# Performance work log

Measured on AMD Instinct MI355X. Metric: run time of the kernel, lower is better.

The kernel has to match this reference:

```python
import jax, jax.numpy as jnp
import numpy as np

B, C, P, D = 4096, 1000, 10, 256
N = C * P            # total prototypes
E = 160000           # edges among prototypes
MARGIN = -0.1
LOSS_WEIGHT = 0.1
EPS = 1e-12          # F.normalize eps


def _gcn_conv(x, src, dst, deg_isqrt, w, b):
    # PyG GCNConv: symmetric-normalized aggregation with self-loops (added by caller)
    xw = x @ w                                   # [N, D]
    norm = deg_isqrt[src] * deg_isqrt[dst]       # [E+N]
    msg = norm[:, None] * xw[src]                # [E+N, D]
    out = jax.ops.segment_sum(msg, dst, num_segments=N)
    return out + b


def setup_inputs() -> dict:
    key = jax.random.key(0)
    ks = jax.random.split(key, 8)
    return {
        "hidden": jax.random.normal(ks[0], (B, D), jnp.float32),
        "labels": jax.random.randint(ks[1], (B,), 0, C),
        "edge_index": jax.random.randint(ks[2], (2, E), 0, N),
        "node_features": 0.02 * jax.random.normal(ks[3], (N, D), jnp.float32),
        "w1": jax.random.normal(ks[4], (D, D), jnp.float32) / np.sqrt(D),
        "b1": jnp.zeros((D,), jnp.float32),
        "w2": jax.random.normal(ks[5], (D, D), jnp.float32) / np.sqrt(D),
        "b2": jnp.zeros((D,), jnp.float32),
    }


def reference(hidden, labels, edge_index, node_features, w1, b1, w2, b2):
    # --- PrototypeGCN over the prototype graph (self-loops + sym norm) ---
    loops = jnp.arange(N, dtype=edge_index.dtype)
    src = jnp.concatenate([edge_index[0], loops])
    dst = jnp.concatenate([edge_index[1], loops])
    deg = jax.ops.segment_sum(jnp.ones_like(dst, jnp.float32), dst, num_segments=N)
    deg_isqrt = jnp.where(deg > 0, jax.lax.rsqrt(jnp.maximum(deg, 1.0)), 0.0)
    x = node_features
    x = jax.nn.relu(_gcn_conv(x, src, dst, deg_isqrt, w1, b1))
    x = jax.nn.relu(_gcn_conv(x, src, dst, deg_isqrt, w2, b2))

    # --- cosine similarity, per-class max over prototypes ---
    hidden_norm = hidden / jnp.maximum(jnp.linalg.norm(hidden, axis=1, keepdims=True), EPS)
    proto_norm = x / jnp.maximum(jnp.linalg.norm(x, axis=1, keepdims=True), EPS)
    sim = (1.0 + hidden_norm @ proto_norm.T) / 2.0          # [B, N]
    sim_pc = sim.reshape(B, C, P)
    output = sim_pc.max(axis=2)                              # [B, C]
    topk_idx = sim_pc.argmax(axis=2)                         # [B, C]

    # --- margin-masked cross entropy ---
    ar = jnp.arange(B)
    true_scores = output[ar, labels]
    pred_labels = output.argmax(axis=1)
    pred_scores = output.max(axis=1)
    mask = (true_scores - pred_scores) > MARGIN              # [B] bool
    cnt = mask.sum()
    per_ce = -jax.nn.log_softmax(output, axis=1)[ar, labels]
    ce_loss = jnp.sum(per_ce * mask) / jnp.maximum(cnt, 1).astype(per_ce.dtype)

    # dispersion = -mean(proto_norm @ proto_norm.T) = -||sum_i p_i||^2 / N^2
    s = proto_norm.sum(axis=0)
    dispersion_loss = -(s @ s) / (N * N)
    total_loss = jnp.where(cnt == 0, 0.0, ce_loss + LOSS_WEIGHT * dispersion_loss)

    # --- vectorized usage scatter (replaces Python double loop) ---
    pos_ids = labels * P + topk_idx[ar, labels]
    positive_usage = jnp.zeros((N,), jnp.float32).at[pos_ids].add(1.0)
    wrong = (pred_labels != labels).astype(jnp.float32)
    neg_ids = pred_labels * P + topk_idx[ar, pred_labels]
    negative_usage = jnp.zeros((N,), jnp.float32).at[neg_ids].add(wrong)

    return (output, total_loss, positive_usage, negative_usage)
```

## Files before the change

### kernel.cpp

```cpp
#include <hip/hip_runtime.h>
#include <math.h>

#define B_  4096
#define C_  1000
#define P_  10
#define D_  256
#define N_  10000
#define E_  160000

typedef __attribute__((ext_vector_type(8))) short short8;
typedef __attribute__((ext_vector_type(4))) float floatx4;

#define MFMA16(a, b, c) __builtin_amdgcn_mfma_f32_16x16x32_bf16((a), (b), (c), 0, 0, 0)

__device__ __forceinline__ float waveReduceSum(float v){
  #pragma unroll
  for (int o = 32; o > 0; o >>= 1) v += __shfl_xor(v, o);
  return v;
}
__device__ __forceinline__ unsigned short f2bf(float f){
  unsigned int u = __float_as_uint(f);
  unsigned int r = (u + 0x7FFFu + ((u >> 16) & 1u)) >> 16;
  return (unsigned short)r;
}
__device__ __forceinline__ float bf2f(unsigned short b){
  return __uint_as_float(((unsigned int)b) << 16);
}
__device__ __forceinline__ void gload_lds16(const void* g, void* l){
  __builtin_amdgcn_global_load_lds((const __attribute__((address_space(1))) void*)g,
                                   (__attribute__((address_space(3))) void*)l, 16, 0, 0);
}

__global__ void k_prep(const int* __restrict__ src, const int* __restrict__ dst,
                       int* __restrict__ cursor, int* __restrict__ csr_src,
                       const float* __restrict__ w1, const float* __restrict__ w2,
                       unsigned short* __restrict__ w1h, unsigned short* __restrict__ w1l,
                       unsigned short* __restrict__ w2h, unsigned short* __restrict__ w2l,
                       float* __restrict__ zero_zone,
                       const float* __restrict__ nodef,
                       unsigned short* __restrict__ NFh, unsigned short* __restrict__ NFl,
                       const float* __restrict__ hidden,
                       unsigned short* __restrict__ HNh, unsigned short* __restrict__ HNl){
  int b = blockIdx.x;
  int t = threadIdx.x;
  if (b < 625){
    int e = b * 256 + t;
    if (e < E_){
      int d = dst[e];
      int p = atomicAdd(&cursor[d], 1);
      p = (p < 63) ? p : 63;
      csr_src[d * 64 + p] = src[e];
    }
  } else if (b < 1137){
    int bb = b - 625;
    const float* w = (bb < 256) ? w1 : w2;
    int n = bb & 255;
    float x = w[(size_t)t * 256 + n];
    unsigned short h = f2bf(x);
    unsigned short l = f2bf(x - bf2f(h));
    if (bb < 256){ w1h[(size_t)n * 256 + t] = h; w1l[(size_t)n * 256 + t] = l; }
    else         { w2h[(size_t)n * 256 + t] = h; w2l[(size_t)n * 256 + t] = l; }
  } else if (b < 1216){
    int i = (b - 1137) * 256 + t;
    if (i < 1 + 2 * N_) zero_zone[i] = 0.f;
  } else if (b < 11216){
    size_t i = (size_t)(b - 1216) * 256 + t;
    float x = nodef[i];
    unsigned short h = f2bf(x);
    NFh[i] = h;
    NFl[i] = f2bf(x - bf2f(h));
  } else {
    int r = b - 11216;
    float v = hidden[(size_t)r * 256 + t];
    float ss = waveReduceSum(v * v);
    __shared__ float red[4];
    int w = t >> 6;
    if ((t & 63) == 0) red[w] = ss;
    __syncthreads();
    float tot = red[0] + red[1] + red[2] + red[3];
    float nrm = fmaxf(sqrtf(tot), 1e-12f);
    float x = v / nrm;
    unsigned short h = f2bf(x);
    HNh[(size_t)r * 256 + t] = h;
    HNl[(size_t)r * 256 + t] = f2bf(x - bf2f(h));
  }
}

__global__ __launch_bounds__(64) void k_gemm_mfma(
    const unsigned short* __restrict__ Ah, const unsigned short* __restrict__ Al,
    const unsigned short* __restrict__ Wh, const unsigned short* __restrict__ Wl,
    float* __restrict__ outp){
  int lane = threadIdx.x;
  int l15 = lane & 15, lq = lane >> 4;
  int rb = blockIdx.x * 64;
  int nb = blockIdx.y * 32;

  floatx4 acc[4][2];
  #pragma unroll
  for (int mt = 0; mt < 4; ++mt)
    #pragma unroll
    for (int nt = 0; nt < 2; ++nt) acc[mt][nt] = (floatx4){0.f,0.f,0.f,0.f};

  int arow[4];
  #pragma unroll
  for (int mt = 0; mt < 4; ++mt){
    int r = rb + mt * 16 + l15;
    arow[mt] = (r < N_) ? r : (N_ - 1);
  }
  for (int kc = 0; kc < 256; kc += 32){
    short8 ah[4], al[4], bh[2], bl[2];
    #pragma unroll
    for (int mt = 0; mt < 4; ++mt){
      size_t o = (size_t)arow[mt] * 256 + kc + lq * 8;
      ah[mt] = *(const short8*)(Ah + o);
      al[mt] = *(const short8*)(Al + o);
    }
    #pragma unroll
    for (int nt = 0; nt < 2; ++nt){
      size_t o = (size_t)(nb + nt * 16 + l15) * 256 + kc + lq * 8;
      bh[nt] = *(const short8*)(Wh + o);
      bl[nt] = *(const short8*)(Wl + o);
    }
    #pragma unroll
    for (int nt = 0; nt < 2; ++nt)
      #pragma unroll
      for (int mt = 0; mt < 4; ++mt) acc[mt][nt] = MFMA16(al[mt], bh[nt], acc[mt][nt]);
    #pragma unroll
    for (int nt = 0; nt < 2; ++nt)
      #pragma unroll
      for (int mt = 0; mt < 4; ++mt) acc[mt][nt] = MFMA16(ah[mt], bl[nt], acc[mt][nt]);
    #pragma unroll
    for (int nt = 0; nt < 2; ++nt)
      #pragma unroll
      for (int mt = 0; mt < 4; ++mt) acc[mt][nt] = MFMA16(ah[mt], bh[nt], acc[mt][nt]);
  }
  #pragma unroll
  for (int mt = 0; mt < 4; ++mt)
    #pragma unroll
    for (int r = 0; r < 4; ++r){
      int row = rb + mt * 16 + lq * 4 + r;
      if (row < N_){
        #pragma unroll
        for (int nt = 0; nt < 2; ++nt)
          outp[(size_t)row * 256 + nb + nt * 16 + l15] = acc[mt][nt][r];
      }
    }
}

__global__ void k_agg_split(const float* __restrict__ XW, const int* __restrict__ deg,
                            const int* __restrict__ csr_src,
                            const float* __restrict__ bias,
                            unsigned short* __restrict__ Xh, unsigned short* __restrict__ Xl){
  int n    = blockIdx.x * 4 + (threadIdx.x >> 6);
  int lane = threadIdx.x & 63;
  int c4   = lane * 4;
  int dgn = deg[n];
  int dg = (dgn < 64) ? dgn : 64;
  int   esr = (lane < dg) ? csr_src[n * 64 + lane] : 0;
  float is  = 1.0f / sqrtf((float)(dgn + 1));
  float en  = (1.0f / sqrtf((float)(deg[esr] + 1))) * is;
  float4 s = *(const float4*)(XW + (size_t)n * 256 + c4);
  float w = is * is;
  float4 a = make_float4(w * s.x, w * s.y, w * s.z, w * s.w);
  int i = 0;
  for (; i + 3 < dg; i += 4){
    int s0 = __shfl(esr, i),   s1 = __shfl(esr, i+1), s2 = __shfl(esr, i+2), s3 = __shfl(esr, i+3);
    float n0 = __shfl(en, i),  n1 = __shfl(en, i+1),  n2 = __shfl(en, i+2),  n3 = __shfl(en, i+3);
    float4 v0 = *(const float4*)(XW + (size_t)s0 * 256 + c4);
    float4 v1 = *(const float4*)(XW + (size_t)s1 * 256 + c4);
    float4 v2 = *(const float4*)(XW + (size_t)s2 * 256 + c4);
    float4 v3 = *(const float4*)(XW + (size_t)s3 * 256 + c4);
    a.x += n0*v0.x + n1*v1.x + n2*v2.x + n3*v3.x;
    a.y += n0*v0.y + n1*v1.y + n2*v2.y + n3*v3.y;
    a.z += n0*v0.z + n1*v1.z + n2*v2.z + n3*v3.z;
    a.w += n0*v0.w + n1*v1.w + n2*v2.w + n3*v3.w;
  }
  for (; i < dg; ++i){
    int s0 = __shfl(esr, i); float n0 = __shfl(en, i);
    float4 v0 = *(const float4*)(XW + (size_t)s0 * 256 + c4);
    a.x += n0 * v0.x; a.y += n0 * v0.y; a.z += n0 * v0.z; a.w += n0 * v0.w;
  }
  float4 b = *(const float4*)(bias + c4);
  float x0 = fmaxf(a.x + b.x, 0.f), x1 = fmaxf(a.y + b.y, 0.f);
  float x2 = fmaxf(a.z + b.z, 0.f), x3 = fmaxf(a.w + b.w, 0.f);
  unsigned short h0 = f2bf(x0), h1 = f2bf(x1), h2 = f2bf(x2), h3 = f2bf(x3);
  ushort4 hv = make_ushort4(h0, h1, h2, h3);
  ushort4 lv = make_ushort4(f2bf(x0 - bf2f(h0)), f2bf(x1 - bf2f(h1)),
                            f2bf(x2 - bf2f(h2)), f2bf(x3 - bf2f(h3)));
  *(ushort4*)(Xh + (size_t)n * 256 + c4) = hv;
  *(ushort4*)(Xl + (size_t)n * 256 + c4) = lv;
}

__global__ void k_agg_norm_split(const float* __restrict__ XW, const int* __restrict__ deg,
                                 const int* __restrict__ csr_src,
                                 const float* __restrict__ bias,
                                 unsigned short* __restrict__ Ph, unsigned short* __restrict__ Pl){
  int n    = blockIdx.x * 4 + (threadIdx.x >> 6);
  int lane = threadIdx.x & 63;
  int c4   = lane * 4;
  int dgn = deg[n];
  int dg = (dgn < 64) ? dgn : 64;
  int   esr = (lane < dg) ? csr_src[n * 64 + lane] : 0;
  float is  = 1.0f / sqrtf((float)(dgn + 1));
  float en  = (1.0f / sqrtf((float)(deg[esr] + 1))) * is;
  float4 s = *(const float4*)(XW + (size_t)n * 256 + c4);
  float w = is * is;
  float4 a = make_float4(w * s.x, w * s.y, w * s.z, w * s.w);
  int i = 0;
  for (; i + 3 < dg; i += 4){
    int s0 = __shfl(esr, i),   s1 = __shfl(esr, i+1), s2 = __shfl(esr, i+2), s3 = __shfl(esr, i+3);
    float n0 = __shfl(en, i),  n1 = __shfl(en, i+1),  n2 = __shfl(en, i+2),  n3 = __shfl(en, i+3);
    float4 v0 = *(const float4*)(XW + (size_t)s0 * 256 + c4);
    float4 v1 = *(const float4*)(XW + (size_t)s1 * 256 + c4);
    float4 v2 = *(const float4*)(XW + (size_t)s2 * 256 + c4);
    float4 v3 = *(const float4*)(XW + (size_t)s3 * 256 + c4);
    a.x += n0*v0.x + n1*v1.x + n2*v2.x + n3*v3.x;
    a.y += n0*v0.y + n1*v1.y + n2*v2.y + n3*v3.y;
    a.z += n0*v0.z + n1*v1.z + n2*v2.z + n3*v3.z;
    a.w += n0*v0.w + n1*v1.w + n2*v2.w + n3*v3.w;
  }
  for (; i < dg; ++i){
    int s0 = __shfl(esr, i); float n0 = __shfl(en, i);
    float4 v0 = *(const float4*)(XW + (size_t)s0 * 256 + c4);
    a.x += n0 * v0.x; a.y += n0 * v0.y; a.z += n0 * v0.z; a.w += n0 * v0.w;
  }
  float4 b = *(const float4*)(bias + c4);
  float x0 = fmaxf(a.x + b.x, 0.f), x1 = fmaxf(a.y + b.y, 0.f);
  float x2 = fmaxf(a.z + b.z, 0.f), x3 = fmaxf(a.w + b.w, 0.f);
  float ss = x0*x0 + x1*x1 + x2*x2 + x3*x3;
  float tot = waveReduceSum(ss);
  float nrm = fmaxf(sqrtf(tot), 1e-12f);
  x0 /= nrm; x1 /= nrm; x2 /= nrm; x3 /= nrm;
  unsigned short h0 = f2bf(x0), h1 = f2bf(x1), h2 = f2bf(x2), h3 = f2bf(x3);
  ushort4 hv = make_ushort4(h0, h1, h2, h3);
  ushort4 lv = make_ushort4(f2bf(x0 - bf2f(h0)), f2bf(x1 - bf2f(h1)),
                            f2bf(x2 - bf2f(h2)), f2bf(x3 - bf2f(h3)));
  *(ushort4*)(Ph + (size_t)n * 256 + c4) = hv;
  *(ushort4*)(Pl + (size_t)n * 256 + c4) = lv;
}

__global__ void k_colsum(const unsigned short* __restrict__ hi,
                         const unsigned short* __restrict__ lo,
                         float* __restrict__ s){
  int d = threadIdx.x;
  int r0 = blockIdx.x * 100;
  float acc = 0.f;
  for (int r = r0; r < r0 + 100; ++r)
    acc += bf2f(hi[(size_t)r * 256 + d]) + bf2f(lo[(size_t)r * 256 + d]);
  atomicAdd(&s[d], acc);
}

__global__ __launch_bounds__(256, 4) void k_sim_max(
    const unsigned short* __restrict__ HNh, const unsigned short* __restrict__ HNl,
    const unsigned short* __restrict__ PNh, const unsigned short* __restrict__ PNl,
    float* __restrict__ out, unsigned char* __restrict__ idxb){
  __shared__ __align__(16) char smem[20736];

  int tid  = threadIdx.x;
  int wid  = tid >> 6;
  int lane = tid & 63;
  int l15  = lane & 15, lq = lane >> 4;
  int rbw  = blockIdx.y * 128 + wid * 32;
  int cb80 = blockIdx.x * 80;

  int swz  = (l15 >> 1) & 3;
  int srow = lane >> 2;
  int skq  = (lane & 3) ^ ((lane >> 3) & 3);

  floatx4 acc[2][5];
  #pragma unroll
  for (int mt = 0; mt < 2; ++mt)
    #pragma unroll
    for (int nt = 0; nt < 5; ++nt) acc[mt][nt] = (floatx4){0.f,0.f,0.f,0.f};

  const unsigned short* a0h = HNh + (size_t)(rbw + l15) * 256 + lq * 8;
  const unsigned short* a0l = HNl + (size_t)(rbw + l15) * 256 + lq * 8;

  auto stage1 = [&](int kc, int pb, int c){
    int bsel = (c >= 5) ? 1 : 0;
    int s = c - bsel * 5;
    int row = s * 16 + srow;
    const unsigned short* gp = (bsel ? PNl : PNh)
        + (size_t)(cb80 + row) * 256 + kc + skq * 8;
    char* lp = smem + pb * 10240 + bsel * 5120 + s * 1024;
    gload_lds16(gp, lp);
  };
  auto stageAll = [&](int kc, int pb){
    stage1(kc, pb, wid);
    stage1(kc, pb, wid + 4);
    if (wid < 2) stage1(kc, pb, wid + 8);
  };

  stageAll(0, 0);
  short8 ah[2], al[2];
  #pragma unroll
  for (int mt = 0; mt < 2; ++mt){
    ah[mt] = *(const short8*)(a0h + (size_t)mt * 4096);
    al[mt] = *(const short8*)(a0l + (size_t)mt * 4096);
  }
  __syncthreads();

  int p = 0;
  for (int kc = 0; kc < 256; kc += 32){
    const unsigned short* Bh = (const unsigned short*)(smem + p * 10240);
    const unsigned short* Bl = Bh + 2560;
    short8 ah2[2], al2[2];
    if (kc < 224){
      stageAll(kc + 32, p ^ 1);
      #pragma unroll
      for (int mt = 0; mt < 2; ++mt){
        ah2[mt] = *(const short8*)(a0h + (size_t)mt * 4096 + kc + 32);
        al2[mt] = *(const short8*)(a0l + (size_t)mt * 4096 + kc + 32);
      }
    }
    {
      int r0 = (0 * 16 + l15) * 32 + (lq ^ swz) * 8;
      int r1 = (1 * 16 + l15) * 32 + (lq ^ swz) * 8;
      int r2 = (2 * 16 + l15) * 32 + (lq ^ swz) * 8;
      short8 bh0 = *(const short8*)(Bh + r0), bl0 = *(const short8*)(Bl + r0);
      short8 bh1 = *(const short8*)(Bh + r1), bl1 = *(const short8*)(Bl + r1);
      short8 bh2 = *(const short8*)(Bh + r2), bl2 = *(const short8*)(Bl + r2);
      acc[0][0] = MFMA16(al[0], bh0, acc[0][0]);
      acc[1][0] = MFMA16(al[1], bh0, acc[1][0]);
      acc[0][1] = MFMA16(al[0], bh1, acc[0][1]);
      acc[1][1] = MFMA16(al[1], bh1, acc[1][1]);
      acc[0][2] = MFMA16(al[0], bh2, acc[0][2]);
      acc[1][2] = MFMA16(al[1], bh2, acc[1][2]);
      acc[0][0] = MFMA16(ah[0], bl0, acc[0][0]);
      acc[1][0] = MFMA16(ah[1], bl0, acc[1][0]);
      acc[0][1] = MFMA16(ah[0], bl1, acc[0][1]);
      acc[1][1] = MFMA16(ah[1], bl1, acc[1][1]);
      acc[0][2] = MFMA16(ah[0], bl2, acc[0][2]);
      acc[1][2] = MFMA16(ah[1], bl2, acc[1][2]);
      acc[0][0] = MFMA16(ah[0], bh0, acc[0][0]);
      acc[1][0] = MFMA16(ah[1], bh0, acc[1][0]);
      acc[0][1] = MFMA16(ah[0], bh1, acc[0][1]);
      acc[1][1] = MFMA16(ah[1], bh1, acc[1][1]);
      acc[0][2] = MFMA16(ah[0], bh2, acc[0][2]);
      acc[1][2] = MFMA16(ah[1], bh2, acc[1][2]);
    }
    {
      int r3 = (3 * 16 + l15) * 32 + (lq ^ swz) * 8;
      int r4 = (4 * 16 + l15) * 32 + (lq ^ swz) * 8;
      short8 bh3 = *(const short8*)(Bh + r3), bl3 = *(const short8*)(Bl + r3);
      short8 bh4 = *(const short8*)(Bh + r4), bl4 = *(const short8*)(Bl + r4);
      acc[0][3] = MFMA16(al[0], bh3, acc[0][3]);
      acc[1][3] = MFMA16(al[1], bh3, acc[1][3]);
      acc[0][4] = MFMA16(al[0], bh4, acc[0][4]);
      acc[1][4] = MFMA16(al[1], bh4, acc[1][4]);
      acc[0][3] = MFMA16(ah[0], bl3, acc[0][3]);
      acc[1][3] = MFMA16(ah[1], bl3, acc[1][3]);
      acc[0][4] = MFMA16(ah[0], bl4, acc[0][4]);
      acc[1][4] = MFMA16(ah[1], bl4, acc[1][4]);
      acc[0][3] = MFMA16(ah[0], bh3, acc[0][3]);
      acc[1][3] = MFMA16(ah[1], bh3, acc[1][3]);
      acc[0][4] = MFMA16(ah[0], bh4, acc[0][4]);
      acc[1][4] = MFMA16(ah[1], bh4, acc[1][4]);
    }
    ah[0] = ah2[0]; ah[1] = ah2[1];
    al[0] = al2[0]; al[1] = al2[1];
    __syncthreads();
    p ^= 1;
  }

  float* redw = (float*)smem + wid * 1296;
  #pragma unroll
  for (int mt = 0; mt < 2; ++mt){
    #pragma unroll
    for (int nt = 0; nt < 5; ++nt)
      #pragma unroll
      for (int r = 0; r < 4; ++r)
        redw[(lq * 4 + r) * 81 + nt * 16 + l15] = acc[mt][nt][r];
    int row = lane >> 2;
    int q   = lane & 3;
    const float* basep = redw + row * 81 + q * 20;
    float vs[2]; int is[2];
    #pragma unroll
    for (int cc = 0; cc < 2; ++cc){
      float m = 0.5f * (1.0f + basep[cc * 10]); int mi = 0;
      #pragma unroll
      for (int p2 = 1; p2 < 10; ++p2){
        float v = 0.5f * (1.0f + basep[cc * 10 + p2]);
        if (v > m){ m = v; mi = p2; }
      }
      vs[cc] = m; is[cc] = mi;
    }
    int grow = rbw + mt * 16 + row;
    int gcol = blockIdx.x * 8 + q * 2;
    *(float2*)(out + (size_t)grow * 1000 + gcol) = make_float2(vs[0], vs[1]);
    idxb[(size_t)grow * 1000 + gcol]     = (unsigned char)is[0];
    idxb[(size_t)grow * 1000 + gcol + 1] = (unsigned char)is[1];
  }
}

__global__ void k_row_pass(const float* __restrict__ out, const unsigned char* __restrict__ idxb,
                           const int* __restrict__ labels, int* __restrict__ cnt,
                           float* __restrict__ ce_sum, float* __restrict__ pos_usage,
                           float* __restrict__ neg_usage){
  int b = blockIdx.x * 4 + (threadIdx.x >> 6);
  int lane = threadIdx.x & 63;
  const float* row = out + (size_t)b * 1000;
  float v[16];
  #pragma unroll
  for (int j = 0; j < 4; ++j){
    int f4 = j * 64 + lane;
    if (f4 < 250){
      float4 t = *(const float4*)(row + f4 * 4);
      v[j*4+0] = t.x; v[j*4+1] = t.y; v[j*4+2] = t.z; v[j*4+3] = t.w;
    } else {
      v[j*4+0] = v[j*4+1] = v[j*4+2] = v[j*4+3] = -INFINITY;
    }
  }
  float m = -INFINITY; int mi = 0x7fffffff;
  #pragma unroll
  for (int j = 0; j < 4; ++j)
    #pragma unroll
    for (int k = 0; k < 4; ++k){
      float x = v[j*4+k];
      if (x > m){ m = x; mi = (j * 64 + lane) * 4 + k; }
    }
  #pragma unroll
  for (int o = 32; o > 0; o >>= 1){
    float m2 = __shfl_xor(m, o);
    int   i2 = __shfl_xor(mi, o);
    if (m2 > m || (m2 == m && i2 < mi)){ m = m2; mi = i2; }
  }
  float s = 0.f;
  #pragma unroll
  for (int t = 0; t < 16; ++t) s += __expf(v[t] - m);
  s = waveReduceSum(s);
  if (lane == 0){
    int lab = labels[b];
    float true_score = row[lab];
    float per_ce = m + __logf(s) - true_score;
    bool mask = (true_score - m) > -0.1f;
    if (mask){ atomicAdd(cnt, 1); atomicAdd(ce_sum, per_ce); }
    int pi = idxb[(size_t)b * 1000 + lab];
    atomicAdd(&pos_usage[lab * P_ + pi], 1.f);
    if (mi != lab){
      int ni = idxb[(size_t)b * 1000 + mi];
      atomicAdd(&neg_usage[mi * P_ + ni], 1.f);
    }
  }
}

__global__ void k_finalize(const float* __restrict__ s, const int* __restrict__ cnt,
                           const float* __restrict__ ce_sum, float* __restrict__ loss_out){
  int t = threadIdx.x;
  float v = s[t];
  float ss = waveReduceSum(v * v);
  __shared__ float red[4];
  if ((t & 63) == 0) red[t >> 6] = ss;
  __syncthreads();
  if (t == 0){
    float tot = red[0] + red[1] + red[2] + red[3];
    float disp = -tot / 1.0e8f;
    int c = *cnt;
    float total = (c == 0) ? 0.f
                : (*ce_sum / (float)(c < 1 ? 1 : c) + 0.1f * disp);
    *loss_out = total;
  }
}

extern "C" void kernel_launch(void* const* d_in, const int* in_sizes, int n_in,
                              void* d_out, int out_size, void* d_ws, size_t ws_size,
                              hipStream_t stream){
  const float* hidden = (const float*)d_in[0];
  const int*   labels = (const int*)  d_in[1];
  const int*   eidx   = (const int*)  d_in[2];
  const float* nodef  = (const float*)d_in[3];
  const float* w1     = (const float*)d_in[4];
  const float* b1     = (const float*)d_in[5];
  const float* w2     = (const float*)d_in[6];
  const float* b2     = (const float*)d_in[7];

  float* out       = (float*)d_out;
  float* loss_out  = out + (size_t)B_ * C_;
  float* pos_usage = loss_out + 1;
  float* neg_usage = pos_usage + N_;

  const int* srcp = eidx;
  const int* dstp = eidx + E_;

  char* base = (char*)d_ws;
  size_t off = 0;
  auto alloc = [&](size_t bytes) -> char* {
    char* p = base + off;
    off = (off + bytes + 255) & ~(size_t)255;
    return p;
  };
  int*   cursor  = (int*)  alloc((size_t)N_ * 4);
  float* svec    = (float*)alloc(256 * 4);
  int*   cnt     = (int*)  alloc(4);
  float* ce_sum  = (float*)alloc(4);
  size_t zero_bytes = off;
  int*   csr_src   = (int*)  alloc((size_t)N_ * 64 * 4);
  float* XW        = (float*)alloc((size_t)N_ * 256 * 4);
  unsigned short* NFh = (unsigned short*)alloc((size_t)N_ * 256 * 2);
  unsigned short* NFl = (unsigned short*)alloc((size_t)N_ * 256 * 2);
  unsigned short* Xh  = (unsigned short*)alloc((size_t)N_ * 256 * 2);
  unsigned short* Xl  = (unsigned short*)alloc((size_t)N_ * 256 * 2);
  unsigned short* Ph  = (unsigned short*)alloc((size_t)N_ * 256 * 2);
  unsigned short* Pl  = (unsigned short*)alloc((size_t)N_ * 256 * 2);
  unsigned short* W1h = (unsigned short*)alloc(256 * 256 * 2);
  unsigned short* W1l = (unsigned short*)alloc(256 * 256 * 2);
  unsigned short* W2h = (unsigned short*)alloc(256 * 256 * 2);
  unsigned short* W2l = (unsigned short*)alloc(256 * 256 * 2);
  unsigned short* HNh = (unsigned short*)alloc((size_t)B_ * 256 * 2);
  unsigned short* HNl = (unsigned short*)alloc((size_t)B_ * 256 * 2);
  unsigned char* idxb = (unsigned char*)alloc((size_t)B_ * C_);

  hipMemsetAsync(base, 0, zero_bytes, stream);

  k_prep<<<15312, 256, 0, stream>>>(srcp, dstp, cursor, csr_src,
                                    w1, w2, W1h, W1l, W2h, W2l, loss_out,
                                    nodef, NFh, NFl, hidden, HNh, HNl);

  dim3 ggrid(157, 8);
  k_gemm_mfma<<<ggrid, 64, 0, stream>>>(NFh, NFl, W1h, W1l, XW);
  k_agg_split<<<N_ / 4, 256, 0, stream>>>(XW, cursor, csr_src, b1, Xh, Xl);
  k_gemm_mfma<<<ggrid, 64, 0, stream>>>(Xh, Xl, W2h, W2l, XW);
  k_agg_norm_split<<<N_ / 4, 256, 0, stream>>>(XW, cursor, csr_src, b2, Ph, Pl);

  k_colsum<<<100, 256, 0, stream>>>(Ph, Pl, svec);

  dim3 sgrid(125, 32);
  k_sim_max<<<sgrid, 256, 0, stream>>>(HNh, HNl, Ph, Pl, out, idxb);

  k_row_pass<<<B_ / 4, 256, 0, stream>>>(out, idxb, labels, cnt, ce_sum, pos_usage, neg_usage);
  k_finalize<<<1, 256, 0, stream>>>(svec, cnt, ce_sum, loss_out);
}
```

Baseline: 334.3 us.

## Unroll gather by eight, swizzle sim_max block order, fold colsum into row pass

The aggregation loops now gather eight neighbour rows per iteration into two independent accumulators, so more loads are in flight and the add dependency chain is shorter. k_sim_max moves from a 2D grid to a 1D grid that is remapped into 16x16 block tiles, so blocks running at the same time share prototype and hidden tiles in L2. The launches over the padding range exit early. The separate column-sum kernel is folded into k_row_pass as 100 extra blocks, which removes one launch. The trade-offs are more registers per thread in the aggregation and wasted early-exit blocks in the sim grid.

```diff
diff --git a/kernel.cpp b/kernel.cpp
--- a/kernel.cpp
+++ b/kernel.cpp
@@ -162,24 +162,29 @@
   float4 s = *(const float4*)(XW + (size_t)n * 256 + c4);
   float w = is * is;
   float4 a = make_float4(w * s.x, w * s.y, w * s.z, w * s.w);
+  float4 a2 = make_float4(0.f, 0.f, 0.f, 0.f);
   int i = 0;
-  for (; i + 3 < dg; i += 4){
-    int s0 = __shfl(esr, i),   s1 = __shfl(esr, i+1), s2 = __shfl(esr, i+2), s3 = __shfl(esr, i+3);
-    float n0 = __shfl(en, i),  n1 = __shfl(en, i+1),  n2 = __shfl(en, i+2),  n3 = __shfl(en, i+3);
-    float4 v0 = *(const float4*)(XW + (size_t)s0 * 256 + c4);
-    float4 v1 = *(const float4*)(XW + (size_t)s1 * 256 + c4);
-    float4 v2 = *(const float4*)(XW + (size_t)s2 * 256 + c4);
-    float4 v3 = *(const float4*)(XW + (size_t)s3 * 256 + c4);
-    a.x += n0*v0.x + n1*v1.x + n2*v2.x + n3*v3.x;
-    a.y += n0*v0.y + n1*v1.y + n2*v2.y + n3*v3.y;
-    a.z += n0*v0.z + n1*v1.z + n2*v2.z + n3*v3.z;
-    a.w += n0*v0.w + n1*v1.w + n2*v2.w + n3*v3.w;
+  for (; i + 7 < dg; i += 8){
+    int   si[8]; float ni[8];
+    #pragma unroll
+    for (int j = 0; j < 8; ++j){ si[j] = __shfl(esr, i+j); ni[j] = __shfl(en, i+j); }
+    float4 vv[8];
+    #pragma unroll
+    for (int j = 0; j < 8; ++j) vv[j] = *(const float4*)(XW + (size_t)si[j] * 256 + c4);
+    #pragma unroll
+    for (int j = 0; j < 4; ++j){
+      a.x  += ni[j]   * vv[j].x;   a.y  += ni[j]   * vv[j].y;
+      a.z  += ni[j]   * vv[j].z;   a.w  += ni[j]   * vv[j].w;
+      a2.x += ni[j+4] * vv[j+4].x; a2.y += ni[j+4] * vv[j+4].y;
+      a2.z += ni[j+4] * vv[j+4].z; a2.w += ni[j+4] * vv[j+4].w;
+    }
   }
   for (; i < dg; ++i){
     int s0 = __shfl(esr, i); float n0 = __shfl(en, i);
     float4 v0 = *(const float4*)(XW + (size_t)s0 * 256 + c4);
     a.x += n0 * v0.x; a.y += n0 * v0.y; a.z += n0 * v0.z; a.w += n0 * v0.w;
   }
+  a.x += a2.x; a.y += a2.y; a.z += a2.z; a.w += a2.w;
   float4 b = *(const float4*)(bias + c4);
   float x0 = fmaxf(a.x + b.x, 0.f), x1 = fmaxf(a.y + b.y, 0.f);
   float x2 = fmaxf(a.z + b.z, 0.f), x3 = fmaxf(a.w + b.w, 0.f);
@@ -206,24 +211,29 @@
   float4 s = *(const float4*)(XW + (size_t)n * 256 + c4);
   float w = is * is;
   float4 a = make_float4(w * s.x, w * s.y, w * s.z, w * s.w);
+  float4 a2 = make_float4(0.f, 0.f, 0.f, 0.f);
   int i = 0;
-  for (; i + 3 < dg; i += 4){
-    int s0 = __shfl(esr, i),   s1 = __shfl(esr, i+1), s2 = __shfl(esr, i+2), s3 = __shfl(esr, i+3);
-    float n0 = __shfl(en, i),  n1 = __shfl(en, i+1),  n2 = __shfl(en, i+2),  n3 = __shfl(en, i+3);
-    float4 v0 = *(const float4*)(XW + (size_t)s0 * 256 + c4);
-    float4 v1 = *(const float4*)(XW + (size_t)s1 * 256 + c4);
-    float4 v2 = *(const float4*)(XW + (size_t)s2 * 256 + c4);
-    float4 v3 = *(const float4*)(XW + (size_t)s3 * 256 + c4);
-    a.x += n0*v0.x + n1*v1.x + n2*v2.x + n3*v3.x;
-    a.y += n0*v0.y + n1*v1.y + n2*v2.y + n3*v3.y;
-    a.z += n0*v0.z + n1*v1.z + n2*v2.z + n3*v3.z;
-    a.w += n0*v0.w + n1*v1.w + n2*v2.w + n3*v3.w;
+  for (; i + 7 < dg; i += 8){
+    int   si[8]; float ni[8];
+    #pragma unroll
+    for (int j = 0; j < 8; ++j){ si[j] = __shfl(esr, i+j); ni[j] = __shfl(en, i+j); }
+    float4 vv[8];
+    #pragma unroll
+    for (int j = 0; j < 8; ++j) vv[j] = *(const float4*)(XW + (size_t)si[j] * 256 + c4);
+    #pragma unroll
+    for (int j = 0; j < 4; ++j){
+      a.x  += ni[j]   * vv[j].x;   a.y  += ni[j]   * vv[j].y;
+      a.z  += ni[j]   * vv[j].z;   a.w  += ni[j]   * vv[j].w;
+      a2.x += ni[j+4] * vv[j+4].x; a2.y += ni[j+4] * vv[j+4].y;
+      a2.z += ni[j+4] * vv[j+4].z; a2.w += ni[j+4] * vv[j+4].w;
+    }
   }
   for (; i < dg; ++i){
     int s0 = __shfl(esr, i); float n0 = __shfl(en, i);
     float4 v0 = *(const float4*)(XW + (size_t)s0 * 256 + c4);
     a.x += n0 * v0.x; a.y += n0 * v0.y; a.z += n0 * v0.z; a.w += n0 * v0.w;
   }
+  a.x += a2.x; a.y += a2.y; a.z += a2.z; a.w += a2.w;
   float4 b = *(const float4*)(bias + c4);
   float x0 = fmaxf(a.x + b.x, 0.f), x1 = fmaxf(a.y + b.y, 0.f);
   float x2 = fmaxf(a.z + b.z, 0.f), x3 = fmaxf(a.w + b.w, 0.f);
@@ -239,29 +249,24 @@
   *(ushort4*)(Pl + (size_t)n * 256 + c4) = lv;
 }
 
-__global__ void k_colsum(const unsigned short* __restrict__ hi,
-                         const unsigned short* __restrict__ lo,
-                         float* __restrict__ s){
-  int d = threadIdx.x;
-  int r0 = blockIdx.x * 100;
-  float acc = 0.f;
-  for (int r = r0; r < r0 + 100; ++r)
-    acc += bf2f(hi[(size_t)r * 256 + d]) + bf2f(lo[(size_t)r * 256 + d]);
-  atomicAdd(&s[d], acc);
-}
-
 __global__ __launch_bounds__(256, 4) void k_sim_max(
     const unsigned short* __restrict__ HNh, const unsigned short* __restrict__ HNl,
     const unsigned short* __restrict__ PNh, const unsigned short* __restrict__ PNl,
     float* __restrict__ out, unsigned char* __restrict__ idxb){
   __shared__ __align__(16) char smem[20736];
 
+  int nblk = blockIdx.x;
+  int st = nblk >> 8, wi = nblk & 255;
+  int bx = (st & 7) * 16 + (wi & 15);
+  int by = (st >> 3) * 16 + (wi >> 4);
+  if (bx >= 125) return;
+
   int tid  = threadIdx.x;
   int wid  = tid >> 6;
   int lane = tid & 63;
   int l15  = lane & 15, lq = lane >> 4;
-  int rbw  = blockIdx.y * 128 + wid * 32;
-  int cb80 = blockIdx.x * 80;
+  int rbw  = by * 128 + wid * 32;
+  int cb80 = bx * 80;
 
   int swz  = (l15 >> 1) & 3;
   int srow = lane >> 2;
@@ -386,7 +391,7 @@
       vs[cc] = m; is[cc] = mi;
     }
     int grow = rbw + mt * 16 + row;
-    int gcol = blockIdx.x * 8 + q * 2;
+    int gcol = bx * 8 + q * 2;
     *(float2*)(out + (size_t)grow * 1000 + gcol) = make_float2(vs[0], vs[1]);
     idxb[(size_t)grow * 1000 + gcol]     = (unsigned char)is[0];
     idxb[(size_t)grow * 1000 + gcol + 1] = (unsigned char)is[1];
@@ -396,8 +401,21 @@
 __global__ void k_row_pass(const float* __restrict__ out, const unsigned char* __restrict__ idxb,
                            const int* __restrict__ labels, int* __restrict__ cnt,
                            float* __restrict__ ce_sum, float* __restrict__ pos_usage,
-                           float* __restrict__ neg_usage){
-  int b = blockIdx.x * 4 + (threadIdx.x >> 6);
+                           float* __restrict__ neg_usage,
+                           const unsigned short* __restrict__ Ph,
+                           const unsigned short* __restrict__ Pl,
+                           float* __restrict__ svec){
+  int blk = blockIdx.x;
+  if (blk >= 1024){
+    int t = threadIdx.x;
+    int r0 = (blk - 1024) * 100;
+    float acc = 0.f;
+    for (int rr = r0; rr < r0 + 100; ++rr)
+      acc += bf2f(Ph[(size_t)rr * 256 + t]) + bf2f(Pl[(size_t)rr * 256 + t]);
+    atomicAdd(&svec[t], acc);
+    return;
+  }
+  int b = blk * 4 + (threadIdx.x >> 6);
   int lane = threadIdx.x & 63;
   const float* row = out + (size_t)b * 1000;
   float v[16];
@@ -522,11 +540,9 @@
   k_gemm_mfma<<<ggrid, 64, 0, stream>>>(Xh, Xl, W2h, W2l, XW);
   k_agg_norm_split<<<N_ / 4, 256, 0, stream>>>(XW, cursor, csr_src, b2, Ph, Pl);
 
-  k_colsum<<<100, 256, 0, stream>>>(Ph, Pl, svec);
-
-  dim3 sgrid(125, 32);
-  k_sim_max<<<sgrid, 256, 0, stream>>>(HNh, HNl, Ph, Pl, out, idxb);
-
-  k_row_pass<<<B_ / 4, 256, 0, stream>>>(out, idxb, labels, cnt, ce_sum, pos_usage, neg_usage);
+  k_sim_max<<<4096, 256, 0, stream>>>(HNh, HNl, Ph, Pl, out, idxb);
+
+  k_row_pass<<<1124, 256, 0, stream>>>(out, idxb, labels, cnt, ce_sum,
+                                       pos_usage, neg_usage, Ph, Pl, svec);
   k_finalize<<<1, 256, 0, stream>>>(svec, cnt, ce_sum, loss_out);
 }
```

Measured after the change: 317.9 us, median of 2. 4.9% less time.
